# Performance work log

Measured on AMD Instinct MI355X. Metric: run time of the kernel, lower is better.

The kernel has to match this reference:

```python
import jax, jax.numpy as jnp
import numpy as np

NZ, N_GEN = 128, 10
H1, H2, IMG = 512, 1024, 784
BATCH = 4096


def setup_inputs() -> dict:
    key = jax.random.key(0)
    ks = jax.random.split(key, 5)
    z = jax.random.normal(ks[0], (BATCH, NZ), dtype=jnp.float32)
    g_idx = jax.random.randint(ks[1], (BATCH,), 0, N_GEN)
    # stacked per-generator MLP weights (fan-in scaled init)
    W1 = jax.random.normal(ks[2], (N_GEN, NZ, H1), dtype=jnp.float32) / np.sqrt(NZ)
    b1 = jnp.zeros((N_GEN, H1), dtype=jnp.float32)
    W2 = jax.random.normal(ks[3], (N_GEN, H1, H2), dtype=jnp.float32) / np.sqrt(H1)
    b2 = jnp.zeros((N_GEN, H2), dtype=jnp.float32)
    W3 = jax.random.normal(ks[4], (N_GEN, H2, IMG), dtype=jnp.float32) / np.sqrt(H2)
    b3 = jnp.zeros((N_GEN, IMG), dtype=jnp.float32)
    return {"z": z, "g_idx": g_idx, "W1": W1, "b1": b1, "W2": W2, "b2": b2, "W3": W3, "b3": b3}


def reference(z, g_idx, W1, b1, W2, b2, W3, b3):
    # Run ALL n_gen sub-generators for every sample (as the torch module does),
    # then gather the chosen branch per sample.
    h = jax.nn.relu(jnp.einsum('bz,gzh->bgh', z, W1) + b1)          # [B, G, H1]
    h = jax.nn.relu(jnp.einsum('bgh,ghk->bgk', h, W2) + b2)         # [B, G, H2]
    images = jnp.tanh(jnp.einsum('bgk,gki->bgi', h, W3) + b3)       # [B, G, IMG]
    # images[arange(B), g_idx]
    out = jnp.take_along_axis(images, g_idx[:, None, None], axis=1)[:, 0]  # [B, IMG]
    return out
```

## Files before the change

### kernel.cpp

```cpp
#include <hip/hip_runtime.h>
#include <math.h>

#define NZ    128
#define H1    512
#define H2    1024
#define IMG   784
#define IMGP  896
#define BATCH 4096
#define NGEN  10
#define MPAD  128

typedef _Float16 f16;
typedef __attribute__((ext_vector_type(8))) _Float16 half8;
typedef __attribute__((ext_vector_type(4))) float floatx4;

#define TB1 ((NZ / 64) * (H1 / 64) * NGEN)
#define TB2 ((H1 / 64) * (H2 / 64) * NGEN)
#define TB3 ((H2 / 64) * (IMGP / 64) * NGEN)

__device__ __forceinline__ void cp16(void* l, const void* g) {
    __builtin_amdgcn_global_load_lds((const __attribute__((address_space(1))) void*)g,
                                     (__attribute__((address_space(3))) void*)l, 16, 0, 0);
}

template<int K, int N, int NPAD>
__device__ __forceinline__ void t_tile(int idx, const float* __restrict__ W,
                                       f16* __restrict__ Wt, f16 (*L)[72]) {
    constexpr int KT = K / 64, NT = NPAD / 64;
    const int g  = idx / (KT * NT);
    const int r2 = idx % (KT * NT);
    const int k0 = (r2 % KT) * 64;
    const int n0 = (r2 / KT) * 64;
    const int t = threadIdx.x;
    {
        const int kk0 = t >> 4;
        const int nq  = (t & 15) * 4;
        #pragma unroll
        for (int it = 0; it < 4; ++it) {
            const int kk = kk0 + it * 16;
            float4 v = make_float4(0.f, 0.f, 0.f, 0.f);
            if (n0 + nq < N)
                v = *(const float4*)(W + ((size_t)g * K + (k0 + kk)) * N + n0 + nq);
            L[nq + 0][kk] = (f16)v.x;
            L[nq + 1][kk] = (f16)v.y;
            L[nq + 2][kk] = (f16)v.z;
            L[nq + 3][kk] = (f16)v.w;
        }
    }
    __syncthreads();
    {
        const int nn0 = t >> 3;
        const int kq  = (t & 7) * 8;
        #pragma unroll
        for (int it = 0; it < 2; ++it) {
            const int nn = nn0 + it * 32;
            *(half8*)(Wt + ((size_t)g * NPAD + (n0 + nn)) * K + k0 + kq) =
                *(const half8*)&L[nn][kq];
        }
    }
}

__global__ __launch_bounds__(256)
void prep(const float* __restrict__ W1, const float* __restrict__ W2,
          const float* __restrict__ W3, f16* __restrict__ W1t,
          f16* __restrict__ W2t, f16* __restrict__ W3t,
          const int* __restrict__ g_idx, int* __restrict__ seg,
          int* __restrict__ perm) {
    __shared__ f16 L[64][72];
    __shared__ int lc[NGEN];
    __shared__ int lb[NGEN + 1];
    int bid = blockIdx.x;
    if (bid == 0) {
        const int t = threadIdx.x;
        if (t < NGEN) lc[t] = 0;
        __syncthreads();
        int gv[BATCH / 256];
        #pragma unroll
        for (int i = 0; i < BATCH / 256; ++i) {
            gv[i] = g_idx[t + i * 256];
            atomicAdd(&lc[gv[i]], 1);
        }
        __syncthreads();
        if (t == 0) {
            int s = 0;
            for (int g = 0; g < NGEN; ++g) { lb[g] = s; s += lc[g]; }
            lb[NGEN] = s;
        }
        __syncthreads();
        if (t <= NGEN) seg[t] = lb[t];
        if (t < NGEN) lc[t] = lb[t];
        __syncthreads();
        #pragma unroll
        for (int i = 0; i < BATCH / 256; ++i) {
            int p = atomicAdd(&lc[gv[i]], 1);
            perm[p] = t + i * 256;
        }
        return;
    }
    --bid;
    if (bid < TB1) { t_tile<NZ, H1, H1>(bid, W1, W1t, L); return; }
    bid -= TB1;
    if (bid < TB2) { t_tile<H1, H2, H2>(bid, W2, W2t, L); return; }
    bid -= TB2;
    t_tile<H2, IMG, IMGP>(bid, W3, W3t, L);
}

template<int K, int NOUT, int NPADB, int ACT, int SCATTER, int GATHER>
__global__ __launch_bounds__(256)
void gemm(const f16* __restrict__ Ap, const float* __restrict__ Az,
          const f16* __restrict__ Wt, const float* __restrict__ bias,
          f16* __restrict__ Ch, float* __restrict__ Cout,
          const int* __restrict__ seg, const int* __restrict__ perm) {
    const int g  = blockIdx.z;
    const int s0 = seg[g];
    const int ng = seg[g + 1] - s0;
    const int m0 = blockIdx.x * 64;
    if (m0 >= ng) return;
    const int n0 = blockIdx.y * 128;

    __shared__ f16 As[2][64 * 64];
    __shared__ f16 Bs[2][128 * 64];

    const int tid = threadIdx.x, lane = tid & 63, w = tid >> 6;

    const f16* gb[4]; int lbo[4];
    #pragma unroll
    for (int j = 0; j < 4; ++j) {
        const int r   = w * 32 + j * 8 + (lane >> 3);
        const int swz = ((lane & 7) ^ ((r >> 1) & 7)) * 8;
        gb[j] = Wt + ((size_t)g * NPADB + n0 + r) * K + swz;
        lbo[j] = (w * 32 + j * 8) * 64;
    }

    const f16* ga[2]; const float* gz[2]; int lao[2]; int awo[2];
    #pragma unroll
    for (int j = 0; j < 2; ++j) {
        const int r   = w * 16 + j * 8 + (lane >> 3);
        const int swz = ((lane & 7) ^ ((r >> 1) & 7)) * 8;
        lao[j] = (w * 16 + j * 8) * 64;
        if constexpr (GATHER != 0) {
            const int pr = min(s0 + m0 + r, BATCH - 1);
            gz[j] = Az + (size_t)perm[pr] * K + (lane & 7) * 8;
            awo[j] = r * 64 + swz;
        } else {
            ga[j] = Ap + (size_t)(s0 + m0 + r) * K + swz;
        }
    }

    float4 rz0[2], rz1[2];

    const int wm = (w & 1) * 32, wn = (w >> 1) * 64;
    const int lm = lane & 15, lq = lane >> 4;

    floatx4 acc[2][4] = {};
    constexpr int NT = K / 64;

    #pragma unroll
    for (int j = 0; j < 4; ++j) { cp16(&Bs[0][lbo[j]], gb[j]); gb[j] += 64; }
    if constexpr (GATHER != 0) {
        #pragma unroll
        for (int j = 0; j < 2; ++j) {
            rz0[j] = *(const float4*)(gz[j]);
            rz1[j] = *(const float4*)(gz[j] + 4);
            gz[j] += 64;
            half8 h;
            h[0] = (f16)rz0[j].x; h[1] = (f16)rz0[j].y;
            h[2] = (f16)rz0[j].z; h[3] = (f16)rz0[j].w;
            h[4] = (f16)rz1[j].x; h[5] = (f16)rz1[j].y;
            h[6] = (f16)rz1[j].z; h[7] = (f16)rz1[j].w;
            *(half8*)&As[0][awo[j]] = h;
        }
    } else {
        #pragma unroll
        for (int j = 0; j < 2; ++j) { cp16(&As[0][lao[j]], ga[j]); ga[j] += 64; }
    }
    __syncthreads();

    int cur = 0;
    #pragma unroll
    for (int kc = 0; kc < NT; ++kc) {
        const bool more = (kc + 1 < NT);
        if (more) {
            #pragma unroll
            for (int j = 0; j < 4; ++j) { cp16(&Bs[cur ^ 1][lbo[j]], gb[j]); gb[j] += 64; }
            if constexpr (GATHER != 0) {
                #pragma unroll
                for (int j = 0; j < 2; ++j) {
                    rz0[j] = *(const float4*)(gz[j]);
                    rz1[j] = *(const float4*)(gz[j] + 4);
                    gz[j] += 64;
                }
            } else {
                #pragma unroll
                for (int j = 0; j < 2; ++j) { cp16(&As[cur ^ 1][lao[j]], ga[j]); ga[j] += 64; }
            }
        }
        #pragma unroll
        for (int ks = 0; ks < 2; ++ks) {
            half8 a[2], b[4];
            #pragma unroll
            for (int mt = 0; mt < 2; ++mt) {
                const int r  = wm + mt * 16 + lm;
                const int pq = (ks * 4 + lq) ^ ((r >> 1) & 7);
                a[mt] = *(const half8*)&As[cur][r * 64 + pq * 8];
            }
            #pragma unroll
            for (int nf = 0; nf < 4; ++nf) {
                const int r  = wn + (nf >> 1) * 32 + 2 * lm + (nf & 1);
                const int pq = (ks * 4 + lq) ^ ((r >> 1) & 7);
                b[nf] = *(const half8*)&Bs[cur][r * 64 + pq * 8];
            }
            #pragma unroll
            for (int mt = 0; mt < 2; ++mt)
                #pragma unroll
                for (int nf = 0; nf < 4; ++nf)
                    acc[mt][nf] = __builtin_amdgcn_mfma_f32_16x16x32_f16(
                        a[mt], b[nf], acc[mt][nf], 0, 0, 0);
        }
        if (more) {
            if constexpr (GATHER != 0) {
                #pragma unroll
                for (int j = 0; j < 2; ++j) {
                    half8 h;
                    h[0] = (f16)rz0[j].x; h[1] = (f16)rz0[j].y;
                    h[2] = (f16)rz0[j].z; h[3] = (f16)rz0[j].w;
                    h[4] = (f16)rz1[j].x; h[5] = (f16)rz1[j].y;
                    h[6] = (f16)rz1[j].z; h[7] = (f16)rz1[j].w;
                    *(half8*)&As[cur ^ 1][awo[j]] = h;
                }
            }
            __syncthreads();
            cur ^= 1;
        }
    }

    const int c = n0 + wn + 2 * lm;
    const float* bg = bias + (size_t)g * NOUT;
    const bool in0 = (!SCATTER) || (c < NOUT);
    const bool in1 = (!SCATTER) || (c + 32 < NOUT);
    const float b0 = in0 ? bg[c]      : 0.f;
    const float b1 = in0 ? bg[c + 1]  : 0.f;
    const float b2 = in1 ? bg[c + 32] : 0.f;
    const float b3 = in1 ? bg[c + 33] : 0.f;
    #pragma unroll
    for (int mt = 0; mt < 2; ++mt)
        #pragma unroll
        for (int rr = 0; rr < 4; ++rr) {
            const int gr = m0 + wm + mt * 16 + lq * 4 + rr;
            if (gr >= ng) continue;
            float x0 = acc[mt][0][rr] + b0;
            float x1 = acc[mt][1][rr] + b1;
            float x2 = acc[mt][2][rr] + b2;
            float x3 = acc[mt][3][rr] + b3;
            if (ACT == 0) {
                x0 = fmaxf(x0, 0.f); x1 = fmaxf(x1, 0.f);
                x2 = fmaxf(x2, 0.f); x3 = fmaxf(x3, 0.f);
            } else {
                const float e0 = __expf(2.f * x0);
                const float e1 = __expf(2.f * x1);
                const float e2 = __expf(2.f * x2);
                const float e3 = __expf(2.f * x3);
                x0 = 1.f - 2.f / (e0 + 1.f);
                x1 = 1.f - 2.f / (e1 + 1.f);
                x2 = 1.f - 2.f / (e2 + 1.f);
                x3 = 1.f - 2.f / (e3 + 1.f);
            }
            if (SCATTER) {
                const size_t orow = (size_t)perm[s0 + gr];
                if (in0) *(float2*)&Cout[orow * NOUT + c]      = make_float2(x0, x1);
                if (in1) *(float2*)&Cout[orow * NOUT + c + 32] = make_float2(x2, x3);
            } else {
                union { uint u; f16 h[2]; } o0, o1;
                o0.h[0] = (f16)x0; o0.h[1] = (f16)x1;
                o1.h[0] = (f16)x2; o1.h[1] = (f16)x3;
                *(uint*)&Ch[(size_t)(s0 + gr) * NOUT + c]      = o0.u;
                *(uint*)&Ch[(size_t)(s0 + gr) * NOUT + c + 32] = o1.u;
            }
        }
}

extern "C" void kernel_launch(void* const* d_in, const int* in_sizes, int n_in,
                              void* d_out, int out_size, void* d_ws, size_t ws_size,
                              hipStream_t stream) {
    const float* z    = (const float*)d_in[0];
    const int*   gidx = (const int*)  d_in[1];
    const float* W1   = (const float*)d_in[2];
    const float* b1   = (const float*)d_in[3];
    const float* W2   = (const float*)d_in[4];
    const float* b2   = (const float*)d_in[5];
    const float* W3   = (const float*)d_in[6];
    const float* b3   = (const float*)d_in[7];
    float* out = (float*)d_out;

    char* ws = (char*)d_ws;
    size_t off = 0;
    auto alloc = [&](size_t bytes) { size_t o = off; off = (off + bytes + 255) & ~255ULL; return o; };
    int* seg  = (int*)(ws + alloc((size_t)(NGEN + 1) * 4));
    int* perm = (int*)(ws + alloc((size_t)(BATCH + MPAD) * 4));
    f16* h1p = (f16*)(ws + alloc((size_t)(BATCH + MPAD) * H1 * 2));
    f16* h2p = (f16*)(ws + alloc((size_t)(BATCH + MPAD) * H2 * 2));
    f16* W1t = (f16*)(ws + alloc((size_t)NGEN * H1 * NZ * 2));
    f16* W2t = (f16*)(ws + alloc((size_t)NGEN * H2 * H1 * 2));
    f16* W3t = (f16*)(ws + alloc((size_t)NGEN * IMGP * H2 * 2));

    prep<<<dim3(1 + TB1 + TB2 + TB3), dim3(256), 0, stream>>>(
        W1, W2, W3, W1t, W2t, W3t, gidx, seg, perm);

    gemm<NZ, H1, H1, 0, 0, 1><<<dim3(16, H1 / 128, NGEN), dim3(256), 0, stream>>>(
        nullptr, z, W1t, b1, h1p, nullptr, seg, perm);
    gemm<H1, H2, H2, 0, 0, 0><<<dim3(16, H2 / 128, NGEN), dim3(256), 0, stream>>>(
        h1p, nullptr, W2t, b2, h2p, nullptr, seg, perm);
    gemm<H2, IMG, IMGP, 1, 1, 0><<<dim3(16, IMGP / 128, NGEN), dim3(256), 0, stream>>>(
        h2p, nullptr, W3t, b3, nullptr, out, seg, perm);
}
```

Measured before the change: 183.7 us.

## Shrink GEMM N-tile to 64 and load A fragments directly into registers

The grouped GEMM tile changes from 64x128 to 64x64, so more blocks launch and the grid fills more CUs. The A operand is no longer staged through LDS: each lane loads its MFMA fragment straight from global memory into double-buffered registers, converting fp32 to fp16 in the gather case. The W3 pad shrinks from 896 to 832 columns, cutting wasted padded work. In exchange, each weight tile is reused across fewer rows and A rows are re-read by more blocks, and the per-lane A loads are less coalesced than the previous LDS copy path.

```diff
diff --git a/kernel.cpp b/kernel.cpp
--- a/kernel.cpp
+++ b/kernel.cpp
@@ -5,7 +5,7 @@
 #define H1    512
 #define H2    1024
 #define IMG   784
-#define IMGP  896
+#define IMGP  832
 #define BATCH 4096
 #define NGEN  10
 #define MPAD  128
@@ -116,132 +116,109 @@
     const int ng = seg[g + 1] - s0;
     const int m0 = blockIdx.x * 64;
     if (m0 >= ng) return;
-    const int n0 = blockIdx.y * 128;
-
-    __shared__ f16 As[2][64 * 64];
-    __shared__ f16 Bs[2][128 * 64];
+    const int n0 = blockIdx.y * 64;
+
+    __shared__ f16 Bs[2][64 * 64];
 
     const int tid = threadIdx.x, lane = tid & 63, w = tid >> 6;
 
-    const f16* gb[4]; int lbo[4];
-    #pragma unroll
-    for (int j = 0; j < 4; ++j) {
-        const int r   = w * 32 + j * 8 + (lane >> 3);
-        const int swz = ((lane & 7) ^ ((r >> 1) & 7)) * 8;
-        gb[j] = Wt + ((size_t)g * NPADB + n0 + r) * K + swz;
-        lbo[j] = (w * 32 + j * 8) * 64;
-    }
-
-    const f16* ga[2]; const float* gz[2]; int lao[2]; int awo[2];
+    const f16* gb[2]; int lbo[2];
     #pragma unroll
     for (int j = 0; j < 2; ++j) {
         const int r   = w * 16 + j * 8 + (lane >> 3);
         const int swz = ((lane & 7) ^ ((r >> 1) & 7)) * 8;
-        lao[j] = (w * 16 + j * 8) * 64;
+        gb[j]  = Wt + ((size_t)g * NPADB + n0 + r) * K + swz;
+        lbo[j] = (w * 16 + j * 8) * 64;
+    }
+
+    const int wm = (w & 1) * 32, wn = (w >> 1) * 32;
+    const int lm = lane & 15, lq = lane >> 4;
+
+    const f16*  gA[2];
+    const float* gz[2];
+    #pragma unroll
+    for (int mt = 0; mt < 2; ++mt) {
+        const int row = wm + mt * 16 + lm;
         if constexpr (GATHER != 0) {
-            const int pr = min(s0 + m0 + r, BATCH - 1);
-            gz[j] = Az + (size_t)perm[pr] * K + (lane & 7) * 8;
-            awo[j] = r * 64 + swz;
+            const int pr = min(s0 + m0 + row, BATCH - 1);
+            gz[mt] = Az + (size_t)perm[pr] * K + lq * 8;
         } else {
-            ga[j] = Ap + (size_t)(s0 + m0 + r) * K + swz;
-        }
-    }
-
-    float4 rz0[2], rz1[2];
-
-    const int wm = (w & 1) * 32, wn = (w >> 1) * 64;
-    const int lm = lane & 15, lq = lane >> 4;
-
-    floatx4 acc[2][4] = {};
+            gA[mt] = Ap + (size_t)(s0 + m0 + row) * K + lq * 8;
+        }
+    }
+
+    floatx4 acc[2][2] = {};
     constexpr int NT = K / 64;
-
-    #pragma unroll
-    for (int j = 0; j < 4; ++j) { cp16(&Bs[0][lbo[j]], gb[j]); gb[j] += 64; }
-    if constexpr (GATHER != 0) {
-        #pragma unroll
-        for (int j = 0; j < 2; ++j) {
-            rz0[j] = *(const float4*)(gz[j]);
-            rz1[j] = *(const float4*)(gz[j] + 4);
-            gz[j] += 64;
-            half8 h;
-            h[0] = (f16)rz0[j].x; h[1] = (f16)rz0[j].y;
-            h[2] = (f16)rz0[j].z; h[3] = (f16)rz0[j].w;
-            h[4] = (f16)rz1[j].x; h[5] = (f16)rz1[j].y;
-            h[6] = (f16)rz1[j].z; h[7] = (f16)rz1[j].w;
-            *(half8*)&As[0][awo[j]] = h;
-        }
-    } else {
-        #pragma unroll
-        for (int j = 0; j < 2; ++j) { cp16(&As[0][lao[j]], ga[j]); ga[j] += 64; }
-    }
+    half8 areg[2][2][2];
+
+    #pragma unroll
+    for (int j = 0; j < 2; ++j) { cp16(&Bs[0][lbo[j]], gb[j]); gb[j] += 64; }
+    #pragma unroll
+    for (int mt = 0; mt < 2; ++mt)
+        #pragma unroll
+        for (int ks = 0; ks < 2; ++ks) {
+            if constexpr (GATHER != 0) {
+                const float4 v0 = *(const float4*)(gz[mt] + ks * 32);
+                const float4 v1 = *(const float4*)(gz[mt] + ks * 32 + 4);
+                half8 h;
+                h[0] = (f16)v0.x; h[1] = (f16)v0.y; h[2] = (f16)v0.z; h[3] = (f16)v0.w;
+                h[4] = (f16)v1.x; h[5] = (f16)v1.y; h[6] = (f16)v1.z; h[7] = (f16)v1.w;
+                areg[0][mt][ks] = h;
+            } else {
+                areg[0][mt][ks] = *(const half8*)(gA[mt] + ks * 32);
+            }
+        }
+    if constexpr (GATHER != 0) { gz[0] += 64; gz[1] += 64; }
+    else                       { gA[0] += 64; gA[1] += 64; }
     __syncthreads();
 
-    int cur = 0;
     #pragma unroll
     for (int kc = 0; kc < NT; ++kc) {
-        const bool more = (kc + 1 < NT);
-        if (more) {
-            #pragma unroll
-            for (int j = 0; j < 4; ++j) { cp16(&Bs[cur ^ 1][lbo[j]], gb[j]); gb[j] += 64; }
-            if constexpr (GATHER != 0) {
+        const int cur = kc & 1;
+        if (kc + 1 < NT) {
+            #pragma unroll
+            for (int j = 0; j < 2; ++j) { cp16(&Bs[cur ^ 1][lbo[j]], gb[j]); gb[j] += 64; }
+            #pragma unroll
+            for (int mt = 0; mt < 2; ++mt)
                 #pragma unroll
-                for (int j = 0; j < 2; ++j) {
-                    rz0[j] = *(const float4*)(gz[j]);
-                    rz1[j] = *(const float4*)(gz[j] + 4);
-                    gz[j] += 64;
+                for (int ks = 0; ks < 2; ++ks) {
+                    if constexpr (GATHER != 0) {
+                        const float4 v0 = *(const float4*)(gz[mt] + ks * 32);
+                        const float4 v1 = *(const float4*)(gz[mt] + ks * 32 + 4);
+                        half8 h;
+                        h[0] = (f16)v0.x; h[1] = (f16)v0.y; h[2] = (f16)v0.z; h[3] = (f16)v0.w;
+                        h[4] = (f16)v1.x; h[5] = (f16)v1.y; h[6] = (f16)v1.z; h[7] = (f16)v1.w;
+                        areg[cur ^ 1][mt][ks] = h;
+                    } else {
+                        areg[cur ^ 1][mt][ks] = *(const half8*)(gA[mt] + ks * 32);
+                    }
                 }
-            } else {
-                #pragma unroll
-                for (int j = 0; j < 2; ++j) { cp16(&As[cur ^ 1][lao[j]], ga[j]); ga[j] += 64; }
-            }
+            if constexpr (GATHER != 0) { gz[0] += 64; gz[1] += 64; }
+            else                       { gA[0] += 64; gA[1] += 64; }
         }
         #pragma unroll
         for (int ks = 0; ks < 2; ++ks) {
-            half8 a[2], b[4];
-            #pragma unroll
-            for (int mt = 0; mt < 2; ++mt) {
-                const int r  = wm + mt * 16 + lm;
-                const int pq = (ks * 4 + lq) ^ ((r >> 1) & 7);
-                a[mt] = *(const half8*)&As[cur][r * 64 + pq * 8];
-            }
-            #pragma unroll
-            for (int nf = 0; nf < 4; ++nf) {
-                const int r  = wn + (nf >> 1) * 32 + 2 * lm + (nf & 1);
+            half8 b[2];
+            #pragma unroll
+            for (int nf = 0; nf < 2; ++nf) {
+                const int r  = wn + 2 * lm + nf;
                 const int pq = (ks * 4 + lq) ^ ((r >> 1) & 7);
                 b[nf] = *(const half8*)&Bs[cur][r * 64 + pq * 8];
             }
             #pragma unroll
             for (int mt = 0; mt < 2; ++mt)
                 #pragma unroll
-                for (int nf = 0; nf < 4; ++nf)
+                for (int nf = 0; nf < 2; ++nf)
                     acc[mt][nf] = __builtin_amdgcn_mfma_f32_16x16x32_f16(
-                        a[mt], b[nf], acc[mt][nf], 0, 0, 0);
-        }
-        if (more) {
-            if constexpr (GATHER != 0) {
-                #pragma unroll
-                for (int j = 0; j < 2; ++j) {
-                    half8 h;
-                    h[0] = (f16)rz0[j].x; h[1] = (f16)rz0[j].y;
-                    h[2] = (f16)rz0[j].z; h[3] = (f16)rz0[j].w;
-                    h[4] = (f16)rz1[j].x; h[5] = (f16)rz1[j].y;
-                    h[6] = (f16)rz1[j].z; h[7] = (f16)rz1[j].w;
-                    *(half8*)&As[cur ^ 1][awo[j]] = h;
-                }
-            }
-            __syncthreads();
-            cur ^= 1;
-        }
+                        areg[cur][mt][ks], b[nf], acc[mt][nf], 0, 0, 0);
+        }
+        if (kc + 1 < NT) __syncthreads();
     }
 
     const int c = n0 + wn + 2 * lm;
-    const float* bg = bias + (size_t)g * NOUT;
     const bool in0 = (!SCATTER) || (c < NOUT);
-    const bool in1 = (!SCATTER) || (c + 32 < NOUT);
-    const float b0 = in0 ? bg[c]      : 0.f;
-    const float b1 = in0 ? bg[c + 1]  : 0.f;
-    const float b2 = in1 ? bg[c + 32] : 0.f;
-    const float b3 = in1 ? bg[c + 33] : 0.f;
+    const float b0 = in0 ? bias[(size_t)g * NOUT + c]     : 0.f;
+    const float b1 = in0 ? bias[(size_t)g * NOUT + c + 1] : 0.f;
     #pragma unroll
     for (int mt = 0; mt < 2; ++mt)
         #pragma unroll
@@ -250,31 +227,23 @@
             if (gr >= ng) continue;
             float x0 = acc[mt][0][rr] + b0;
             float x1 = acc[mt][1][rr] + b1;
-            float x2 = acc[mt][2][rr] + b2;
-            float x3 = acc[mt][3][rr] + b3;
             if (ACT == 0) {
                 x0 = fmaxf(x0, 0.f); x1 = fmaxf(x1, 0.f);
-                x2 = fmaxf(x2, 0.f); x3 = fmaxf(x3, 0.f);
             } else {
                 const float e0 = __expf(2.f * x0);
                 const float e1 = __expf(2.f * x1);
-                const float e2 = __expf(2.f * x2);
-                const float e3 = __expf(2.f * x3);
                 x0 = 1.f - 2.f / (e0 + 1.f);
                 x1 = 1.f - 2.f / (e1 + 1.f);
-                x2 = 1.f - 2.f / (e2 + 1.f);
-                x3 = 1.f - 2.f / (e3 + 1.f);
             }
             if (SCATTER) {
-                const size_t orow = (size_t)perm[s0 + gr];
-                if (in0) *(float2*)&Cout[orow * NOUT + c]      = make_float2(x0, x1);
-                if (in1) *(float2*)&Cout[orow * NOUT + c + 32] = make_float2(x2, x3);
+                if (in0) {
+                    const size_t orow = (size_t)perm[s0 + gr];
+                    *(float2*)&Cout[orow * NOUT + c] = make_float2(x0, x1);
+                }
             } else {
-                union { uint u; f16 h[2]; } o0, o1;
-                o0.h[0] = (f16)x0; o0.h[1] = (f16)x1;
-                o1.h[0] = (f16)x2; o1.h[1] = (f16)x3;
-                *(uint*)&Ch[(size_t)(s0 + gr) * NOUT + c]      = o0.u;
-                *(uint*)&Ch[(size_t)(s0 + gr) * NOUT + c + 32] = o1.u;
+                union { uint u; f16 h[2]; } o;
+                o.h[0] = (f16)x0; o.h[1] = (f16)x1;
+                *(uint*)&Ch[(size_t)(s0 + gr) * NOUT + c] = o.u;
             }
         }
 }
@@ -306,10 +275,10 @@
     prep<<<dim3(1 + TB1 + TB2 + TB3), dim3(256), 0, stream>>>(
         W1, W2, W3, W1t, W2t, W3t, gidx, seg, perm);
 
-    gemm<NZ, H1, H1, 0, 0, 1><<<dim3(16, H1 / 128, NGEN), dim3(256), 0, stream>>>(
+    gemm<NZ, H1, H1, 0, 0, 1><<<dim3(16, H1 / 64, NGEN), dim3(256), 0, stream>>>(
         nullptr, z, W1t, b1, h1p, nullptr, seg, perm);
-    gemm<H1, H2, H2, 0, 0, 0><<<dim3(16, H2 / 128, NGEN), dim3(256), 0, stream>>>(
+    gemm<H1, H2, H2, 0, 0, 0><<<dim3(16, H2 / 64, NGEN), dim3(256), 0, stream>>>(
         h1p, nullptr, W2t, b2, h2p, nullptr, seg, perm);
-    gemm<H2, IMG, IMGP, 1, 1, 0><<<dim3(16, IMGP / 128, NGEN), dim3(256), 0, stream>>>(
+    gemm<H2, IMG, IMGP, 1, 1, 0><<<dim3(16, IMGP / 64, NGEN), dim3(256), 0, stream>>>(
         h2p, nullptr, W3t, b3, nullptr, out, seg, perm);
 }
```

New measurement: 253.3 us. 1.38x slower.

## Use 128x128 tiles with deeper cp16 prefetch, XCD swizzle, and specialized layer-1 kernel

Applied to the files above, without the earlier changes.

Replaces the 64x128 grouped GEMM with a 128x128-tile kernel. Each wave now holds a 4x4 MFMA accumulator block, both operand tiles are loaded with async global-to-LDS copies, and a two-stage-ahead prefetch is synchronised with explicit vmcnt waits and barriers. A flat 1D grid is remapped in chunks of eight, apparently to group each generator's tiles on the same XCD and improve L2 reuse of weights. Layer 1 gets its own kernel that gathers and converts all of z up front, since K=128 needs only two k-steps. The larger tiles cut redundant operand loads and barriers per FLOP. In exchange there are fewer workgroups, more register pressure, and more wasted rows per generator segment.

```diff
diff --git a/kernel.cpp b/kernel.cpp
--- a/kernel.cpp
+++ b/kernel.cpp
@@ -105,153 +105,120 @@
     t_tile<H2, IMG, IMGP>(bid, W3, W3t, L);
 }
 
-template<int K, int NOUT, int NPADB, int ACT, int SCATTER, int GATHER>
+template<int K, int NOUT, int NPADB, int NM, int NN, int ACT, int SCATTER>
 __global__ __launch_bounds__(256)
-void gemm(const f16* __restrict__ Ap, const float* __restrict__ Az,
-          const f16* __restrict__ Wt, const float* __restrict__ bias,
-          f16* __restrict__ Ch, float* __restrict__ Cout,
-          const int* __restrict__ seg, const int* __restrict__ perm) {
-    const int g  = blockIdx.z;
+void gemm128(const f16* __restrict__ Ap, const f16* __restrict__ Wt,
+             const float* __restrict__ bias, f16* __restrict__ Ch,
+             float* __restrict__ Cout, const int* __restrict__ seg,
+             const int* __restrict__ perm) {
+    constexpr int NT  = K / 64;
+    constexpr int NWG = NM * NN * NGEN;
+    static_assert(NWG % 8 == 0, "gen-chunk swizzle needs NWG % 8 == 0");
+    static_assert(NT >= 2, "pipeline assumes K >= 128");
+    constexpr int CHUNK = NWG / 8;
+
+    const int H = blockIdx.x;
+    const int L = (H & 7) * CHUNK + (H >> 3);
+    const int g   = L / (NM * NN);
+    const int rem = L - g * (NM * NN);
+    const int nt  = rem / NM;
+    const int mt0 = rem - nt * NM;
     const int s0 = seg[g];
     const int ng = seg[g + 1] - s0;
-    const int m0 = blockIdx.x * 64;
+    const int m0 = mt0 * 128;
     if (m0 >= ng) return;
-    const int n0 = blockIdx.y * 128;
-
-    __shared__ f16 As[2][64 * 64];
-    __shared__ f16 Bs[2][128 * 64];
+    const int n0 = nt * 128;
+
+    __shared__ f16 As[2 * 128 * 64];
+    __shared__ f16 Bs[2 * 128 * 64];
 
     const int tid = threadIdx.x, lane = tid & 63, w = tid >> 6;
 
-    const f16* gb[4]; int lbo[4];
+    const f16* ga[4]; const f16* gb[4]; int lo[4];
     #pragma unroll
     for (int j = 0; j < 4; ++j) {
         const int r   = w * 32 + j * 8 + (lane >> 3);
         const int swz = ((lane & 7) ^ ((r >> 1) & 7)) * 8;
+        ga[j] = Ap + (size_t)(s0 + m0 + r) * K + swz;
         gb[j] = Wt + ((size_t)g * NPADB + n0 + r) * K + swz;
-        lbo[j] = (w * 32 + j * 8) * 64;
-    }
-
-    const f16* ga[2]; const float* gz[2]; int lao[2]; int awo[2];
-    #pragma unroll
-    for (int j = 0; j < 2; ++j) {
-        const int r   = w * 16 + j * 8 + (lane >> 3);
-        const int swz = ((lane & 7) ^ ((r >> 1) & 7)) * 8;
-        lao[j] = (w * 16 + j * 8) * 64;
-        if constexpr (GATHER != 0) {
-            const int pr = min(s0 + m0 + r, BATCH - 1);
-            gz[j] = Az + (size_t)perm[pr] * K + (lane & 7) * 8;
-            awo[j] = r * 64 + swz;
-        } else {
-            ga[j] = Ap + (size_t)(s0 + m0 + r) * K + swz;
-        }
-    }
-
-    float4 rz0[2], rz1[2];
-
-    const int wm = (w & 1) * 32, wn = (w >> 1) * 64;
+        lo[j] = (w * 32 + j * 8) * 64;
+    }
+
+    const int wm = (w & 1) * 64, wn = (w >> 1) * 64;
     const int lm = lane & 15, lq = lane >> 4;
 
-    floatx4 acc[2][4] = {};
-    constexpr int NT = K / 64;
-
-    #pragma unroll
-    for (int j = 0; j < 4; ++j) { cp16(&Bs[0][lbo[j]], gb[j]); gb[j] += 64; }
-    if constexpr (GATHER != 0) {
-        #pragma unroll
-        for (int j = 0; j < 2; ++j) {
-            rz0[j] = *(const float4*)(gz[j]);
-            rz1[j] = *(const float4*)(gz[j] + 4);
-            gz[j] += 64;
-            half8 h;
-            h[0] = (f16)rz0[j].x; h[1] = (f16)rz0[j].y;
-            h[2] = (f16)rz0[j].z; h[3] = (f16)rz0[j].w;
-            h[4] = (f16)rz1[j].x; h[5] = (f16)rz1[j].y;
-            h[6] = (f16)rz1[j].z; h[7] = (f16)rz1[j].w;
-            *(half8*)&As[0][awo[j]] = h;
-        }
-    } else {
-        #pragma unroll
-        for (int j = 0; j < 2; ++j) { cp16(&As[0][lao[j]], ga[j]); ga[j] += 64; }
-    }
-    __syncthreads();
-
-    int cur = 0;
-    #pragma unroll
+    const int c = n0 + wn + 2 * lm;
+    const bool in0 = (!SCATTER) || (c < NOUT);
+    const bool in1 = (!SCATTER) || (c + 32 < NOUT);
+    const float* bg = bias + (size_t)g * NOUT;
+    const float bv0 = in0 ? bg[c]      : 0.f;
+    const float bv1 = in0 ? bg[c + 1]  : 0.f;
+    const float bv2 = in1 ? bg[c + 32] : 0.f;
+    const float bv3 = in1 ? bg[c + 33] : 0.f;
+
+    floatx4 acc[4][4] = {};
+
+    auto stage = [&](int t, int b) {
+        #pragma unroll
+        for (int j = 0; j < 4; ++j) cp16(&As[b * 8192 + lo[j]], ga[j] + (size_t)t * 64);
+        #pragma unroll
+        for (int j = 0; j < 4; ++j) cp16(&Bs[b * 8192 + lo[j]], gb[j] + (size_t)t * 64);
+    };
+    stage(0, 0);
+    __builtin_amdgcn_sched_barrier(0);
+    stage(1, 1);
+
     for (int kc = 0; kc < NT; ++kc) {
-        const bool more = (kc + 1 < NT);
-        if (more) {
-            #pragma unroll
-            for (int j = 0; j < 4; ++j) { cp16(&Bs[cur ^ 1][lbo[j]], gb[j]); gb[j] += 64; }
-            if constexpr (GATHER != 0) {
-                #pragma unroll
-                for (int j = 0; j < 2; ++j) {
-                    rz0[j] = *(const float4*)(gz[j]);
-                    rz1[j] = *(const float4*)(gz[j] + 4);
-                    gz[j] += 64;
-                }
-            } else {
-                #pragma unroll
-                for (int j = 0; j < 2; ++j) { cp16(&As[cur ^ 1][lao[j]], ga[j]); ga[j] += 64; }
-            }
-        }
+        if (kc + 1 < NT) asm volatile("s_waitcnt vmcnt(8)" ::: "memory");
+        else             asm volatile("s_waitcnt vmcnt(0)" ::: "memory");
+        __builtin_amdgcn_sched_barrier(0);
+        __builtin_amdgcn_s_barrier();
+        __builtin_amdgcn_sched_barrier(0);
+
+        const int cb = (kc & 1) * 8192;
+        half8 a[2][4], b[2][4];
         #pragma unroll
         for (int ks = 0; ks < 2; ++ks) {
-            half8 a[2], b[4];
-            #pragma unroll
-            for (int mt = 0; mt < 2; ++mt) {
+            #pragma unroll
+            for (int mt = 0; mt < 4; ++mt) {
                 const int r  = wm + mt * 16 + lm;
                 const int pq = (ks * 4 + lq) ^ ((r >> 1) & 7);
-                a[mt] = *(const half8*)&As[cur][r * 64 + pq * 8];
+                a[ks][mt] = *(const half8*)&As[cb + r * 64 + pq * 8];
             }
             #pragma unroll
             for (int nf = 0; nf < 4; ++nf) {
                 const int r  = wn + (nf >> 1) * 32 + 2 * lm + (nf & 1);
                 const int pq = (ks * 4 + lq) ^ ((r >> 1) & 7);
-                b[nf] = *(const half8*)&Bs[cur][r * 64 + pq * 8];
-            }
-            #pragma unroll
-            for (int mt = 0; mt < 2; ++mt)
+                b[ks][nf] = *(const half8*)&Bs[cb + r * 64 + pq * 8];
+            }
+        }
+        asm volatile("s_waitcnt lgkmcnt(0)" ::: "memory");
+        __builtin_amdgcn_sched_barrier(0);
+        if (kc + 2 < NT) {
+            __builtin_amdgcn_s_barrier();
+            __builtin_amdgcn_sched_barrier(0);
+            stage(kc + 2, kc & 1);
+        }
+        #pragma unroll
+        for (int ks = 0; ks < 2; ++ks)
+            #pragma unroll
+            for (int mt = 0; mt < 4; ++mt)
                 #pragma unroll
                 for (int nf = 0; nf < 4; ++nf)
                     acc[mt][nf] = __builtin_amdgcn_mfma_f32_16x16x32_f16(
-                        a[mt], b[nf], acc[mt][nf], 0, 0, 0);
-        }
-        if (more) {
-            if constexpr (GATHER != 0) {
-                #pragma unroll
-                for (int j = 0; j < 2; ++j) {
-                    half8 h;
-                    h[0] = (f16)rz0[j].x; h[1] = (f16)rz0[j].y;
-                    h[2] = (f16)rz0[j].z; h[3] = (f16)rz0[j].w;
-                    h[4] = (f16)rz1[j].x; h[5] = (f16)rz1[j].y;
-                    h[6] = (f16)rz1[j].z; h[7] = (f16)rz1[j].w;
-                    *(half8*)&As[cur ^ 1][awo[j]] = h;
-                }
-            }
-            __syncthreads();
-            cur ^= 1;
-        }
-    }
-
-    const int c = n0 + wn + 2 * lm;
-    const float* bg = bias + (size_t)g * NOUT;
-    const bool in0 = (!SCATTER) || (c < NOUT);
-    const bool in1 = (!SCATTER) || (c + 32 < NOUT);
-    const float b0 = in0 ? bg[c]      : 0.f;
-    const float b1 = in0 ? bg[c + 1]  : 0.f;
-    const float b2 = in1 ? bg[c + 32] : 0.f;
-    const float b3 = in1 ? bg[c + 33] : 0.f;
-    #pragma unroll
-    for (int mt = 0; mt < 2; ++mt)
+                        a[ks][mt], b[ks][nf], acc[mt][nf], 0, 0, 0);
+    }
+
+    #pragma unroll
+    for (int mt = 0; mt < 4; ++mt)
         #pragma unroll
         for (int rr = 0; rr < 4; ++rr) {
             const int gr = m0 + wm + mt * 16 + lq * 4 + rr;
             if (gr >= ng) continue;
-            float x0 = acc[mt][0][rr] + b0;
-            float x1 = acc[mt][1][rr] + b1;
-            float x2 = acc[mt][2][rr] + b2;
-            float x3 = acc[mt][3][rr] + b3;
+            float x0 = acc[mt][0][rr] + bv0;
+            float x1 = acc[mt][1][rr] + bv1;
+            float x2 = acc[mt][2][rr] + bv2;
+            float x3 = acc[mt][3][rr] + bv3;
             if (ACT == 0) {
                 x0 = fmaxf(x0, 0.f); x1 = fmaxf(x1, 0.f);
                 x2 = fmaxf(x2, 0.f); x3 = fmaxf(x3, 0.f);
@@ -279,6 +246,114 @@
         }
 }
 
+__global__ __launch_bounds__(256)
+void gemm_l1(const float* __restrict__ Az, const f16* __restrict__ Wt,
+             const float* __restrict__ bias, f16* __restrict__ Ch,
+             const int* __restrict__ seg, const int* __restrict__ perm) {
+    constexpr int K = NZ, NOUT = H1, NPADB = H1, NM = 8, NN = 4;
+    constexpr int NWG = NM * NN * NGEN, CHUNK = NWG / 8;
+    const int H = blockIdx.x;
+    const int L = (H & 7) * CHUNK + (H >> 3);
+    const int g   = L / (NM * NN);
+    const int rem = L - g * (NM * NN);
+    const int nt  = rem / NM;
+    const int mt0 = rem - nt * NM;
+    const int s0 = seg[g];
+    const int ng = seg[g + 1] - s0;
+    const int m0 = mt0 * 128;
+    if (m0 >= ng) return;
+    const int n0 = nt * 128;
+
+    __shared__ f16 As[2 * 8192];
+    __shared__ f16 Bs[2 * 8192];
+    const int tid = threadIdx.x, lane = tid & 63, w = tid >> 6;
+
+    #pragma unroll
+    for (int j = 0; j < 4; ++j) {
+        const int r   = w * 32 + j * 8 + (lane >> 3);
+        const int swz = ((lane & 7) ^ ((r >> 1) & 7)) * 8;
+        const f16* gbj = Wt + ((size_t)g * NPADB + n0 + r) * K + swz;
+        const int  loj = (w * 32 + j * 8) * 64;
+        cp16(&Bs[loj],        gbj);
+        cp16(&Bs[8192 + loj], gbj + 64);
+    }
+    int prow[4];
+    #pragma unroll
+    for (int p = 0; p < 4; ++p) {
+        const int r = w * 32 + p * 8 + (lane >> 3);
+        prow[p] = perm[min(s0 + m0 + r, BATCH - 1)];
+    }
+    #pragma unroll
+    for (int t = 0; t < 2; ++t)
+        #pragma unroll
+        for (int p = 0; p < 4; ++p) {
+            const int r = w * 32 + p * 8 + (lane >> 3);
+            const float* src = Az + (size_t)prow[p] * K + t * 64 + (lane & 7) * 8;
+            const float4 v0 = *(const float4*)src;
+            const float4 v1 = *(const float4*)(src + 4);
+            half8 h;
+            h[0] = (f16)v0.x; h[1] = (f16)v0.y; h[2] = (f16)v0.z; h[3] = (f16)v0.w;
+            h[4] = (f16)v1.x; h[5] = (f16)v1.y; h[6] = (f16)v1.z; h[7] = (f16)v1.w;
+            const int pq = (lane & 7) ^ ((r >> 1) & 7);
+            *(half8*)&As[t * 8192 + r * 64 + pq * 8] = h;
+        }
+
+    const int wm = (w & 1) * 64, wn = (w >> 1) * 64;
+    const int lm = lane & 15, lq = lane >> 4;
+    const int c = n0 + wn + 2 * lm;
+    const float* bg = bias + (size_t)g * NOUT;
+    const float bv0 = bg[c], bv1 = bg[c + 1], bv2 = bg[c + 32], bv3 = bg[c + 33];
+
+    __syncthreads();
+
+    floatx4 acc[4][4] = {};
+    #pragma unroll
+    for (int kc = 0; kc < 2; ++kc) {
+        const int cb = kc * 8192;
+        half8 a[2][4], b[2][4];
+        #pragma unroll
+        for (int ks = 0; ks < 2; ++ks) {
+            #pragma unroll
+            for (int mt = 0; mt < 4; ++mt) {
+                const int r  = wm + mt * 16 + lm;
+                const int pq = (ks * 4 + lq) ^ ((r >> 1) & 7);
+                a[ks][mt] = *(const half8*)&As[cb + r * 64 + pq * 8];
+            }
+            #pragma unroll
+            for (int nf = 0; nf < 4; ++nf) {
+                const int r  = wn + (nf >> 1) * 32 + 2 * lm + (nf & 1);
+                const int pq = (ks * 4 + lq) ^ ((r >> 1) & 7);
+                b[ks][nf] = *(const half8*)&Bs[cb + r * 64 + pq * 8];
+            }
+        }
+        #pragma unroll
+        for (int ks = 0; ks < 2; ++ks)
+            #pragma unroll
+            for (int mt = 0; mt < 4; ++mt)
+                #pragma unroll
+                for (int nf = 0; nf < 4; ++nf)
+                    acc[mt][nf] = __builtin_amdgcn_mfma_f32_16x16x32_f16(
+                        a[ks][mt], b[ks][nf], acc[mt][nf], 0, 0, 0);
+    }
+
+    #pragma unroll
+    for (int mt = 0; mt < 4; ++mt)
+        #pragma unroll
+        for (int rr = 0; rr < 4; ++rr) {
+            const int gr = m0 + wm + mt * 16 + lq * 4 + rr;
+            if (gr >= ng) continue;
+            float x0 = fmaxf(acc[mt][0][rr] + bv0, 0.f);
+            float x1 = fmaxf(acc[mt][1][rr] + bv1, 0.f);
+            float x2 = fmaxf(acc[mt][2][rr] + bv2, 0.f);
+            float x3 = fmaxf(acc[mt][3][rr] + bv3, 0.f);
+            union { uint u; f16 h[2]; } o0, o1;
+            o0.h[0] = (f16)x0; o0.h[1] = (f16)x1;
+            o1.h[0] = (f16)x2; o1.h[1] = (f16)x3;
+            *(uint*)&Ch[(size_t)(s0 + gr) * NOUT + c]      = o0.u;
+            *(uint*)&Ch[(size_t)(s0 + gr) * NOUT + c + 32] = o1.u;
+        }
+}
+
 extern "C" void kernel_launch(void* const* d_in, const int* in_sizes, int n_in,
                               void* d_out, int out_size, void* d_ws, size_t ws_size,
                               hipStream_t stream) {
@@ -306,10 +381,10 @@
     prep<<<dim3(1 + TB1 + TB2 + TB3), dim3(256), 0, stream>>>(
         W1, W2, W3, W1t, W2t, W3t, gidx, seg, perm);
 
-    gemm<NZ, H1, H1, 0, 0, 1><<<dim3(16, H1 / 128, NGEN), dim3(256), 0, stream>>>(
-        nullptr, z, W1t, b1, h1p, nullptr, seg, perm);
-    gemm<H1, H2, H2, 0, 0, 0><<<dim3(16, H2 / 128, NGEN), dim3(256), 0, stream>>>(
-        h1p, nullptr, W2t, b2, h2p, nullptr, seg, perm);
-    gemm<H2, IMG, IMGP, 1, 1, 0><<<dim3(16, IMGP / 128, NGEN), dim3(256), 0, stream>>>(
-        h2p, nullptr, W3t, b3, nullptr, out, seg, perm);
-}
+    gemm_l1<<<dim3(8 * 4 * NGEN), dim3(256), 0, stream>>>(
+        z, W1t, b1, h1p, seg, perm);
+    gemm128<H1, H2, H2, 8, 8, 0, 0><<<dim3(8 * 8 * NGEN), dim3(256), 0, stream>>>(
+        h1p, W2t, b2, h2p, nullptr, seg, perm);
+    gemm128<H2, IMG, IMGP, 8, 7, 1, 1><<<dim3(8 * 7 * NGEN), dim3(256), 0, stream>>>(
+        h2p, W3t, b3, nullptr, out, seg, perm);
+}
```

New measurement: 155.4 us. 1.18x faster.
